# Kernel optimization log

Hardware: AMD Instinct MI355X
Metric: run time of the kernel (lower is better)

Reference implementation:

```python
import jax, jax.numpy as jnp
import numpy as np

N, B, D, T = 128, 512, 128, 16  # regions, batch, embed_dim, decode steps
C_CLIP = 10.0                   # tanh_clipping
NEG = -1e9


def setup_inputs() -> dict:
    key = jax.random.key(0)
    ks = jax.random.split(key, 40)
    s = 1.0 / np.sqrt(D)

    def w(k, shape):
        return jax.random.uniform(k, shape, jnp.float32, -s, s)

    return {
        'data': jax.random.normal(ks[0], (N, B, 4), jnp.float32),
        'node_embed': w(ks[1], (4, D)),
        'init_placeholder': w(ks[2], (D,)),
        'W1_w': w(ks[3], (D, D)), 'W1_b': w(ks[4], (D,)),
        'W2_w': w(ks[5], (D, D)), 'W2_b': w(ks[6], (D,)),
        'W3_w': w(ks[7], (D, D)), 'W3_b': w(ks[8], (D,)),
        'agg1_w': w(ks[9], (D, D)), 'agg1_b': w(ks[10], (D,)),
        'agg2_w': w(ks[11], (D, D)), 'agg2_b': w(ks[12], (D,)),
        'agg3_w': w(ks[13], (D, D)), 'agg3_b': w(ks[14], (D,)),
        'r1': jnp.ones((1,), jnp.float32),
        'r2': jnp.ones((1,), jnp.float32),
        'r3': jnp.ones((1,), jnp.float32),
        'lstm_Wih': w(ks[15], (4 * D, D)), 'lstm_Whh': w(ks[16], (4 * D, D)),
        'lstm_bih': w(ks[17], (4 * D,)), 'lstm_bhh': w(ks[18], (4 * D,)),
        'ptr_Wq': w(ks[19], (D, D)), 'ptr_bq': w(ks[20], (D,)),
        'ptr_Wref': w(ks[21], (D, D)), 'ptr_bref': w(ks[22], (D,)),
        'ptr_v': w(ks[23], (D,)),
        'glm_Wq': w(ks[24], (D, D)), 'glm_bq': w(ks[25], (D,)),
        'glm_Wref': w(ks[26], (D, D)), 'glm_bref': w(ks[27], (D,)),
        'glm_v': w(ks[28], (D,)),
    }


def _lin(x, w, b):
    return x @ w.T + b


def _attn_logits(q, e, Wq, bq, v):
    # q: [B,D], e: [B,D,N] (1x1-conv-projected ref). Bahdanau: v . tanh(Wq q + e)
    qq = (q @ Wq.T + bq)[:, :, None]          # [B,D,1]
    return jnp.einsum('d,bdn->bn', v, jnp.tanh(qq + e))  # [B,N]


def reference(data, node_embed, init_placeholder,
              W1_w, W1_b, W2_w, W2_b, W3_w, W3_b,
              agg1_w, agg1_b, agg2_w, agg2_b, agg3_w, agg3_b,
              r1, r2, r3,
              lstm_Wih, lstm_Whh, lstm_bih, lstm_bhh,
              ptr_Wq, ptr_bq, ptr_Wref, ptr_bref, ptr_v,
              glm_Wq, glm_bq, glm_Wref, glm_bref, glm_v):
    # node embedding: [N,B,4] @ [4,D] -> [N,B,D]
    emb = jnp.einsum('nbf,fd->nbd', data, node_embed)
    # GPN graph context: gated local transform + aggregated mean over nodes
    ctx = r1 * _lin(emb, W1_w, W1_b) + (1.0 - r1) * jax.nn.relu(_lin(emb.mean(0), agg1_w, agg1_b))
    ctx = r2 * _lin(ctx, W2_w, W2_b) + (1.0 - r2) * jax.nn.relu(_lin(ctx.mean(0), agg2_w, agg2_b))
    ctx = r3 * _lin(ctx, W3_w, W3_b) + (1.0 - r3) * jax.nn.relu(_lin(ctx.mean(0), agg3_w, agg3_b))
    # precompute 1x1-conv ref projections (ref is fixed over decode steps): [B,D,N]
    e_ptr = jnp.einsum('oi,nbi->bon', ptr_Wref, ctx) + ptr_bref[None, :, None]
    e_glm = jnp.einsum('oi,nbi->bon', glm_Wref, ctx) + glm_bref[None, :, None]
    emb_bnd = emb.transpose(1, 0, 2)  # [B,N,D] for gathering next decoder input

    def step(carry, _):
        h, c, x, visited = carry
        # LSTMCell (torch gate order i,f,g,o)
        gates = x @ lstm_Wih.T + lstm_bih + h @ lstm_Whh.T + lstm_bhh
        i, f, g, o = jnp.split(gates, 4, axis=-1)
        c = jax.nn.sigmoid(f) * c + jax.nn.sigmoid(i) * jnp.tanh(g)
        h = jax.nn.sigmoid(o) * jnp.tanh(c)
        # one glimpse (use_tanh=False), masked
        lg = _attn_logits(h, e_glm, glm_Wq, glm_bq, glm_v)
        lg = jnp.where(visited, NEG, lg)
        gl = jnp.einsum('bdn,bn->bd', e_glm, jax.nn.softmax(lg, axis=-1))
        # pointer (use_tanh=True, C=10), masked
        lp = C_CLIP * jnp.tanh(_attn_logits(gl, e_ptr, ptr_Wq, ptr_bq, ptr_v))
        lp = jnp.where(visited, NEG, lp)
        log_p = jax.nn.log_softmax(lp, axis=-1)  # temp = 1.0
        sel = jnp.argmax(log_p, axis=-1)         # greedy decode, [B]
        visited = visited | jax.nn.one_hot(sel, N, dtype=bool)
        x = jnp.take_along_axis(emb_bnd, sel[:, None, None], axis=1)[:, 0]  # [B,D]
        return (h, c, x, visited), log_p

    h0 = jnp.zeros((B, D), emb.dtype)
    c0 = jnp.zeros((B, D), emb.dtype)
    x0 = jnp.broadcast_to(init_placeholder, (B, D)).astype(emb.dtype)
    visited0 = jnp.zeros((B, N), bool)
    _, log_ps = jax.lax.scan(step, (h0, c0, x0, visited0), None, length=T)
    return log_ps  # [T,B,N]
```

## Files before the change

### kernel.cpp

```cpp
#include <hip/hip_runtime.h>
#include <math.h>


#define NREG   128
#define BATCH  512
#define DIM    128
#define TSTEPS 16
#define NEGV   (-1e9f)
#define LOG2E  1.4426950408889634f
#define CT     2.8853900817779268f

__device__ __forceinline__ float fexp2(float x) { return __builtin_amdgcn_exp2f(x); }
__device__ __forceinline__ float frcp(float x)  { return __builtin_amdgcn_rcpf(x); }
__device__ __forceinline__ float fast_tanh(float x) {
    return 1.f - 2.f * frcp(1.f + fexp2(CT * x));
}
__device__ __forceinline__ float fast_sig(float x) {
    return frcp(1.f + fexp2(-LOG2E * x));
}
__device__ __forceinline__ float fast_exp(float x) { return fexp2(LOG2E * x); }
__device__ __forceinline__ float fast_log(float x) {
    return __builtin_amdgcn_logf(x) * 0.6931471805599453f;
}

__device__ __forceinline__ float dot128(const float* __restrict__ wrow,
                                        const float* __restrict__ s) {
    float a0 = 0.f, a1 = 0.f, a2 = 0.f, a3 = 0.f;
#pragma unroll
    for (int k = 0; k < 128; k += 4) {
        a0 += wrow[k] * s[k];         a1 += wrow[k + 1] * s[k + 1];
        a2 += wrow[k + 2] * s[k + 2]; a3 += wrow[k + 3] * s[k + 3];
    }
    return (a0 + a1) + (a2 + a3);
}

__global__ __launch_bounds__(256) void k_misc(
    const float* __restrict__ Whh, const float* __restrict__ gWq,
    const float* __restrict__ Wih, const float* __restrict__ NE,
    const float* __restrict__ init_ph,
    const float* __restrict__ bih, const float* __restrict__ bhh,
    const float* __restrict__ W1, const float* __restrict__ b1,
    const float* __restrict__ W2, const float* __restrict__ b2,
    const float* __restrict__ W3, const float* __restrict__ b3,
    const float* __restrict__ a1w, const float* __restrict__ a1b,
    const float* __restrict__ a2w, const float* __restrict__ a2b,
    const float* __restrict__ a3w, const float* __restrict__ a3b,
    const float* __restrict__ gWr, const float* __restrict__ gbr,
    const float* __restrict__ pWr, const float* __restrict__ pbr,
    const float* __restrict__ pWq, const float* __restrict__ pbq,
    const float* __restrict__ r1p, const float* __restrict__ r2p,
    const float* __restrict__ r3p,
    const float* __restrict__ pv, const float* __restrict__ data,
    float* __restrict__ WhhP, float* __restrict__ gWqP,
    float* __restrict__ WihNE4, float* __restrict__ g0,
    float* __restrict__ bc, float* __restrict__ sumvp,
    float* __restrict__ Qgc, float* __restrict__ Qpc, float* __restrict__ GPQ,
    float* __restrict__ og, float* __restrict__ op, float* __restrict__ pog)
{
    __shared__ float Ws[128 * 129];
    __shared__ float me[1024], Cv[1024], Mv[1024], Tv[1024], C2[1024], M2[1024];
    __shared__ float NEs[512], mdS[32];
    __shared__ float4 Uc[128], Vc[128], Qgu[128];

    const int blk = blockIdx.x, t = threadIdx.x;

    if (blk < 64) {
        int idx = blk * 256 + t;
        int kb = idx >> 9, g = idx & 511;
        float4 v = *(const float4*)(Whh + g * 128 + kb * 4);
        ((float4*)WhhP)[kb * 512 + g] = v;
    } else if (blk < 80) {
        int idx = (blk - 64) * 256 + t;
        int ib = idx >> 7, o = idx & 127;
        float4 v = *(const float4*)(gWq + o * 128 + ib * 4);
        ((float4*)gWqP)[ib * 128 + o] = v;
    } else if (blk < 82) {
        int g = (blk - 80) * 256 + t;
        float a0 = 0.f, a1 = 0.f, a2 = 0.f, a3 = 0.f;
        for (int d = 0; d < 128; d += 4) {
            float4 wv = *(const float4*)(Wih + g * 128 + d);
            float4 n0 = *(const float4*)(NE + 0 * 128 + d);
            float4 n1 = *(const float4*)(NE + 1 * 128 + d);
            float4 n2 = *(const float4*)(NE + 2 * 128 + d);
            float4 n3 = *(const float4*)(NE + 3 * 128 + d);
            a0 += wv.x * n0.x + wv.y * n0.y + wv.z * n0.z + wv.w * n0.w;
            a1 += wv.x * n1.x + wv.y * n1.y + wv.z * n1.z + wv.w * n1.w;
            a2 += wv.x * n2.x + wv.y * n2.y + wv.z * n2.z + wv.w * n2.w;
            a3 += wv.x * n3.x + wv.y * n3.y + wv.z * n3.z + wv.w * n3.w;
        }
        *(float4*)(WihNE4 + g * 4) = make_float4(a0, a1, a2, a3);
    } else if (blk == 82) {
        for (int g = t; g < 512; g += 256) {
            float acc = 0.f;
            for (int d = 0; d < 128; d += 4) {
                float4 wv = *(const float4*)(Wih + g * 128 + d);
                float4 iv = *(const float4*)(init_ph + d);
                acc += wv.x * iv.x + wv.y * iv.y + wv.z * iv.z + wv.w * iv.w;
            }
            g0[g] = acc;
            bc[g] = bih[g] + bhh[g];
        }
        if (t < 64) {
            float sv = pv[t] + pv[t + 64];
            for (int off = 32; off; off >>= 1) sv += __shfl_xor(sv, off, 64);
            if (t == 0) sumvp[0] = sv;
        }
    } else if (blk == 83) {
        if (t < 128)
            Uc[t] = make_float4(NE[t], NE[128 + t], NE[256 + t], NE[384 + t]);
        __syncthreads();
#define CH_STAGE(Wp, SRC, DST, SC)                                             \
        if (t < 128) {                                                         \
            const float* wr = (Wp) + t * 128;                                  \
            float ax = 0.f, ay = 0.f, az = 0.f, aw = 0.f;                      \
            _Pragma("unroll 8")                                                \
            for (int k = 0; k < 128; k++) {                                    \
                float w = wr[k]; float4 u = SRC[k];                            \
                ax += w * u.x; ay += w * u.y; az += w * u.z; aw += w * u.w;    \
            }                                                                  \
            float sc = (SC);                                                   \
            DST[t] = make_float4(sc * ax, sc * ay, sc * az, sc * aw);          \
        }                                                                      \
        __syncthreads();
        CH_STAGE(W1, Uc, Vc, r1p[0])
        CH_STAGE(W2, Vc, Uc, r2p[0])
        CH_STAGE(W3, Uc, Vc, r3p[0])
        CH_STAGE(gWr, Vc, Qgu, 1.f)
        CH_STAGE(pWr, Vc, Uc, 1.f)
        CH_STAGE(pWq, Qgu, Vc, 1.f)
        if (t < 128) {
            float4 qg = Qgu[t], qp = Uc[t];
            ((float4*)Qgc)[t] = make_float4(CT * qg.x, CT * qg.y, CT * qg.z, CT * qg.w);
            ((float4*)Qpc)[t] = make_float4(CT * qp.x, CT * qp.y, CT * qp.z, CT * qp.w);
            ((float4*)GPQ)[t] = Vc[t];
        }
#undef CH_STAGE
    } else {
        const int b0 = (blk - 84) * 8;
        const float r1 = r1p[0], r2 = r2p[0], r3 = r3p[0];
#define STAGE_W(Wptr)                                                          \
        for (int i = t * 4; i < 16384; i += 1024) {                            \
            float4 v = *(const float4*)((Wptr) + i);                           \
            int oo = i >> 7, kk = i & 127;                                     \
            float* p = &Ws[oo * 129 + kk];                                     \
            p[0] = v.x; p[1] = v.y; p[2] = v.z; p[3] = v.w;                    \
        }
        if (t < 32) {
            int j = t >> 2, f = t & 3;
            float acc = 0.f;
            for (int n = 0; n < 128; n++) acc += data[n * 2048 + (b0 + j) * 4 + f];
            mdS[t] = acc * (1.f / 128.f);
        }
        for (int i = t; i < 512; i += 256) NEs[i] = NE[i];
        __syncthreads();
        for (int idx = t; idx < 1024; idx += 256) {
            int j = idx >> 7, d = idx & 127;
            me[idx] = mdS[j * 4 + 0] * NEs[d] + mdS[j * 4 + 1] * NEs[128 + d] +
                      mdS[j * 4 + 2] * NEs[256 + d] + mdS[j * 4 + 3] * NEs[384 + d];
        }
        STAGE_W(a1w);
        __syncthreads();
        {
            int o = t & 127, jg = t >> 7;
            for (int jj = 0; jj < 4; jj++) {
                int j = jg * 4 + jj;
                float acc = dot128(&Ws[o * 129], &me[j * 128]);
                Tv[j * 128 + o] = (1.f - r1) * fmaxf(acc + a1b[o], 0.f);
            }
        }
        __syncthreads();
        STAGE_W(W1);
        for (int idx = t; idx < 1024; idx += 256) Cv[idx] = r1 * b1[idx & 127] + Tv[idx];
        __syncthreads();
        {
            int o = t & 127, jg = t >> 7;
            for (int jj = 0; jj < 4; jj++) {
                int j = jg * 4 + jj;
                float acc = dot128(&Ws[o * 129], &me[j * 128]);
                Mv[j * 128 + o] = r1 * (acc + b1[o]) + Tv[j * 128 + o];
            }
        }
        __syncthreads();
        STAGE_W(a2w);
        __syncthreads();
        {
            int o = t & 127, jg = t >> 7;
            for (int jj = 0; jj < 4; jj++) {
                int j = jg * 4 + jj;
                float acc = dot128(&Ws[o * 129], &Mv[j * 128]);
                Tv[j * 128 + o] = (1.f - r2) * fmaxf(acc + a2b[o], 0.f);
            }
        }
        __syncthreads();
        STAGE_W(W2);
        __syncthreads();
        {
            int o = t & 127, jg = t >> 7;
            for (int jj = 0; jj < 4; jj++) {
                int j = jg * 4 + jj;
                float ac = dot128(&Ws[o * 129], &Cv[j * 128]);
                float am = dot128(&Ws[o * 129], &Mv[j * 128]);
                C2[j * 128 + o] = r2 * (ac + b2[o]) + Tv[j * 128 + o];
                M2[j * 128 + o] = r2 * (am + b2[o]) + Tv[j * 128 + o];
            }
        }
        __syncthreads();
        STAGE_W(a3w);
        __syncthreads();
        {
            int o = t & 127, jg = t >> 7;
            for (int jj = 0; jj < 4; jj++) {
                int j = jg * 4 + jj;
                float acc = dot128(&Ws[o * 129], &M2[j * 128]);
                Tv[j * 128 + o] = (1.f - r3) * fmaxf(acc + a3b[o], 0.f);
            }
        }
        __syncthreads();
        STAGE_W(W3);
        __syncthreads();
        {
            int o = t & 127, jg = t >> 7;
            for (int jj = 0; jj < 4; jj++) {
                int j = jg * 4 + jj;
                float acc = dot128(&Ws[o * 129], &C2[j * 128]);
                Cv[j * 128 + o] = r3 * (acc + b3[o]) + Tv[j * 128 + o];
            }
        }
        __syncthreads();
        STAGE_W(gWr);
        __syncthreads();
        {
            int o = t & 127, jg = t >> 7;
            for (int jj = 0; jj < 4; jj++) {
                int j = jg * 4 + jj;
                float acc = dot128(&Ws[o * 129], &Cv[j * 128]) + gbr[o];
                Mv[j * 128 + o] = acc;
                og[(long)(b0 + j) * 128 + o] = acc;
            }
        }
        __syncthreads();
        STAGE_W(pWr);
        __syncthreads();
        {
            int o = t & 127, jg = t >> 7;
            for (int jj = 0; jj < 4; jj++) {
                int j = jg * 4 + jj;
                op[(long)(b0 + j) * 128 + o] = dot128(&Ws[o * 129], &Cv[j * 128]) + pbr[o];
            }
        }
        __syncthreads();
        STAGE_W(pWq);
        __syncthreads();
        {
            int o = t & 127, jg = t >> 7;
            for (int jj = 0; jj < 4; jj++) {
                int j = jg * 4 + jj;
                pog[(long)(b0 + j) * 128 + o] = dot128(&Ws[o * 129], &Mv[j * 128]) + pbq[o];
            }
        }
#undef STAGE_W
    }
}

__global__ __launch_bounds__(512, 4) void k_decode(
    const float* __restrict__ dataIn,
    const float* __restrict__ WhhP,
    const float* __restrict__ gWqP,
    const float* __restrict__ WihNE4,
    const float* __restrict__ g0,
    const float* __restrict__ bc,
    const float* __restrict__ Qgc, const float* __restrict__ Qpc,
    const float* __restrict__ GPQ,
    const float* __restrict__ ogG, const float* __restrict__ opG,
    const float* __restrict__ pogG,
    const float* __restrict__ gbq, const float* __restrict__ vgG,
    const float* __restrict__ vpG, const float* __restrict__ sumvpG,
    float* __restrict__ out)
{
    __shared__ float4 dataS[128];
    __shared__ float4 WihS[512];
    __shared__ float4 QgcS[128], QpcS[128], GPQS[128];
    __shared__ float g0S[512], bcS[512], gatesS[512];
    __shared__ float ogS[128], opS[128], pogS[128];
    __shared__ float gbqS[128], vg2S[128], vp2S[128];
    __shared__ float hS[128], cS[128], qeS[128], qepS[128];
    __shared__ float lpart[4][128];
    __shared__ int   visitedS[128];
    __shared__ int   selS;
    __shared__ float sumvpS;

    const int t = threadIdx.x;
    const int b = blockIdx.x;

    if (t < 128) {
        dataS[t] = *(const float4*)(dataIn + ((long)t * 512 + b) * 4);
        QgcS[t]  = ((const float4*)Qgc)[t];
        QpcS[t]  = ((const float4*)Qpc)[t];
        GPQS[t]  = ((const float4*)GPQ)[t];
        ogS[t]   = ogG[(long)b * 128 + t];
        opS[t]   = opG[(long)b * 128 + t];
        pogS[t]  = pogG[(long)b * 128 + t];
        gbqS[t]  = gbq[t];
        vg2S[t]  = -2.f * vgG[t];
        vp2S[t]  = -2.f * vpG[t];
        hS[t] = 0.f; cS[t] = 0.f;
        visitedS[t] = 0;
    }
    WihS[t] = ((const float4*)WihNE4)[t];
    g0S[t] = g0[t];
    bcS[t] = bc[t];
    if (t == 0) sumvpS = sumvpG[0];
    __syncthreads();

    for (int step = 0; step < TSTEPS; step++) {
        {
            float ihp;
            if (step == 0) {
                ihp = g0S[t];
            } else {
                float4 xd = dataS[selS];
                float4 w = WihS[t];
                ihp = xd.x * w.x + xd.y * w.y + xd.z * w.z + xd.w * w.w;
            }
            ihp += bcS[t];
            const float4* wp = (const float4*)WhhP + t;
            float a0 = 0.f, a1 = 0.f, a2 = 0.f, a3 = 0.f;
#pragma unroll 8
            for (int kb = 0; kb < 32; kb++) {
                float4 w = wp[kb * 512];
                a0 += w.x * hS[4 * kb];     a1 += w.y * hS[4 * kb + 1];
                a2 += w.z * hS[4 * kb + 2]; a3 += w.w * hS[4 * kb + 3];
            }
            gatesS[t] = ihp + (a0 + a1) + (a2 + a3);
        }
        __syncthreads();
        if (t < 128) {
            float ig  = fast_sig(gatesS[t]);
            float fg  = fast_sig(gatesS[128 + t]);
            float gg  = fast_tanh(gatesS[256 + t]);
            float og_ = fast_sig(gatesS[384 + t]);
            float cn = fg * cS[t] + ig * gg;
            cS[t] = cn;
            hS[t] = og_ * fast_tanh(cn);
        }
        __syncthreads();
        if (t < 128) {
            const float4* wp = (const float4*)gWqP + t;
            float a0 = 0.f, a1 = 0.f, a2 = 0.f, a3 = 0.f;
#pragma unroll 8
            for (int ib = 0; ib < 32; ib++) {
                float4 w = wp[ib * 128];
                a0 += w.x * hS[4 * ib];     a1 += w.y * hS[4 * ib + 1];
                a2 += w.z * hS[4 * ib + 2]; a3 += w.w * hS[4 * ib + 3];
            }
            float q = (a0 + a1) + (a2 + a3) + gbqS[t];
            qeS[t] = CT * (q + ogS[t]);
        }
        __syncthreads();
        {
            int n = t & 127, q4 = t >> 7, d0 = q4 * 32;
            float4 dn = dataS[n];
            float acc = 0.f;
#pragma unroll 8
            for (int j = 0; j < 32; j++) {
                int d = d0 + j;
                float4 qg = QgcS[d];
                float x = qeS[d] + dn.x * qg.x + dn.y * qg.y + dn.z * qg.z + dn.w * qg.w;
                acc += vg2S[d] * frcp(1.f + fexp2(x));
            }
            lpart[q4][n] = acc;
        }
        __syncthreads();
        if (t < 64) {
            float l0 = visitedS[t] ? NEGV
                     : (lpart[0][t] + lpart[1][t]) + (lpart[2][t] + lpart[3][t]);
            float l1 = visitedS[t + 64] ? NEGV
                     : (lpart[0][t + 64] + lpart[1][t + 64]) + (lpart[2][t + 64] + lpart[3][t + 64]);
            float m = fmaxf(l0, l1);
            for (int off = 32; off; off >>= 1) m = fmaxf(m, __shfl_xor(m, off, 64));
            float p0 = fast_exp(l0 - m), p1 = fast_exp(l1 - m);
            float s = p0 + p1;
            float4 d0v = dataS[t], d1v = dataS[t + 64];
            float q0 = p0 * d0v.x + p1 * d1v.x;
            float q1 = p0 * d0v.y + p1 * d1v.y;
            float q2 = p0 * d0v.z + p1 * d1v.z;
            float q3 = p0 * d0v.w + p1 * d1v.w;
            for (int off = 32; off; off >>= 1) {
                s  += __shfl_xor(s, off, 64);
                q0 += __shfl_xor(q0, off, 64);
                q1 += __shfl_xor(q1, off, 64);
                q2 += __shfl_xor(q2, off, 64);
                q3 += __shfl_xor(q3, off, 64);
            }
            float inv = frcp(s);
            q0 *= inv; q1 *= inv; q2 *= inv; q3 *= inv;
            float4 gA = GPQS[t];
            qepS[t] = CT * (q0 * gA.x + q1 * gA.y + q2 * gA.z + q3 * gA.w
                            + pogS[t] + opS[t]);
            float4 gB = GPQS[t + 64];
            qepS[t + 64] = CT * (q0 * gB.x + q1 * gB.y + q2 * gB.z + q3 * gB.w
                                 + pogS[t + 64] + opS[t + 64]);
        }
        __syncthreads();
        {
            int n = t & 127, q4 = t >> 7, d0 = q4 * 32;
            float4 dn = dataS[n];
            float acc = 0.f;
#pragma unroll 8
            for (int j = 0; j < 32; j++) {
                int d = d0 + j;
                float4 qp = QpcS[d];
                float x = qepS[d] + dn.x * qp.x + dn.y * qp.y + dn.z * qp.z + dn.w * qp.w;
                acc += vp2S[d] * frcp(1.f + fexp2(x));
            }
            lpart[q4][n] = acc;
        }
        __syncthreads();
        if (t < 64) {
            float s0 = sumvpS + (lpart[0][t] + lpart[1][t]) + (lpart[2][t] + lpart[3][t]);
            float s1 = sumvpS + (lpart[0][t + 64] + lpart[1][t + 64])
                              + (lpart[2][t + 64] + lpart[3][t + 64]);
            float l0 = visitedS[t]      ? NEGV : 10.f * fast_tanh(s0);
            float l1 = visitedS[t + 64] ? NEGV : 10.f * fast_tanh(s1);
            float m = fmaxf(l0, l1);
            for (int off = 32; off; off >>= 1) m = fmaxf(m, __shfl_xor(m, off, 64));
            float p0 = fast_exp(l0 - m), p1 = fast_exp(l1 - m);
            float s = p0 + p1;
            for (int off = 32; off; off >>= 1) s += __shfl_xor(s, off, 64);
            float lse = m + fast_log(s);
            float* outp = out + ((long)step * BATCH + b) * NREG;
            outp[t] = l0 - lse;
            outp[t + 64] = l1 - lse;
            float v; int idx;
            if (l1 > l0) { v = l1; idx = t + 64; } else { v = l0; idx = t; }
            for (int off = 32; off; off >>= 1) {
                float ov = __shfl_xor(v, off, 64);
                int   oi = __shfl_xor(idx, off, 64);
                if (ov > v || (ov == v && oi < idx)) { v = ov; idx = oi; }
            }
            if (t == 0) { selS = idx; visitedS[idx] = 1; }
        }
        __syncthreads();
    }
}

extern "C" void kernel_launch(void* const* d_in, const int* in_sizes, int n_in,
                              void* d_out, int out_size, void* d_ws, size_t ws_size,
                              hipStream_t stream) {
    const float* data = (const float*)d_in[0];
    const float* NE   = (const float*)d_in[1];
    const float* init = (const float*)d_in[2];
    const float* W1w = (const float*)d_in[3];  const float* W1b = (const float*)d_in[4];
    const float* W2w = (const float*)d_in[5];  const float* W2b = (const float*)d_in[6];
    const float* W3w = (const float*)d_in[7];  const float* W3b = (const float*)d_in[8];
    const float* A1w = (const float*)d_in[9];  const float* A1b = (const float*)d_in[10];
    const float* A2w = (const float*)d_in[11]; const float* A2b = (const float*)d_in[12];
    const float* A3w = (const float*)d_in[13]; const float* A3b = (const float*)d_in[14];
    const float* r1  = (const float*)d_in[15];
    const float* r2  = (const float*)d_in[16];
    const float* r3  = (const float*)d_in[17];
    const float* Wih = (const float*)d_in[18]; const float* Whh = (const float*)d_in[19];
    const float* bih = (const float*)d_in[20]; const float* bhh = (const float*)d_in[21];
    const float* pWq = (const float*)d_in[22]; const float* pbq = (const float*)d_in[23];
    const float* pWr = (const float*)d_in[24]; const float* pbr = (const float*)d_in[25];
    const float* pv  = (const float*)d_in[26];
    const float* gWq = (const float*)d_in[27]; const float* gbq = (const float*)d_in[28];
    const float* gWr = (const float*)d_in[29]; const float* gbr = (const float*)d_in[30];
    const float* gv  = (const float*)d_in[31];
    float* out = (float*)d_out;

    float* ws     = (float*)d_ws;
    float* WhhP   = ws;
    float* gWqP   = WhhP + 65536;
    float* WihNE4 = gWqP + 16384;
    float* g0     = WihNE4 + 2048;
    float* bc     = g0 + 512;
    float* Qgc    = bc + 512;
    float* Qpc    = Qgc + 512;
    float* GPQ    = Qpc + 512;
    float* og     = GPQ + 512;
    float* op     = og + 65536;
    float* pog    = op + 65536;
    float* sumvp  = pog + 65536;

    k_misc<<<148, 256, 0, stream>>>(Whh, gWq, Wih, NE, init, bih, bhh,
                                    W1w, W1b, W2w, W2b, W3w, W3b,
                                    A1w, A1b, A2w, A2b, A3w, A3b,
                                    gWr, gbr, pWr, pbr, pWq, pbq,
                                    r1, r2, r3, pv, data,
                                    WhhP, gWqP, WihNE4, g0, bc, sumvp,
                                    Qgc, Qpc, GPQ, og, op, pog);
    k_decode<<<BATCH, 512, 0, stream>>>(data, WhhP, gWqP, WihNE4, g0, bc,
                                        Qgc, Qpc, GPQ, og, op, pog,
                                        gbq, gv, pv, sumvp, out);
}
```

Baseline: 366.5 us.

## Double decode block size and split LSTM and query matvecs across more threads

The decode kernel now launches 1024 threads per block instead of 512. The LSTM hidden matvec is split so each pair of threads handles half of a gate row, combined with a shuffle. The glimpse query matvec now uses 512 threads, four per output, reduced with shuffles, instead of 128. The aim is to shorten the serial per-step matvec latency by adding parallelism. In exchange there are more idle threads in the other phases, heavier __syncthreads, and the launch bound of 1024 with 8 blocks may force register pressure or limit occupancy.

```diff
diff --git a/kernel.cpp b/kernel.cpp
--- a/kernel.cpp
+++ b/kernel.cpp
@@ -262,7 +262,7 @@
     }
 }
 
-__global__ __launch_bounds__(512, 4) void k_decode(
+__global__ __launch_bounds__(1024, 8) void k_decode(
     const float* __restrict__ dataIn,
     const float* __restrict__ WhhP,
     const float* __restrict__ gWqP,
@@ -280,7 +280,7 @@
     __shared__ float4 dataS[128];
     __shared__ float4 WihS[512];
     __shared__ float4 QgcS[128], QpcS[128], GPQS[128];
-    __shared__ float g0S[512], bcS[512], gatesS[512];
+    __shared__ float g0S[512], bcS[512], gateS[512];
     __shared__ float ogS[128], opS[128], pogS[128];
     __shared__ float gbqS[128], vg2S[128], vp2S[128];
     __shared__ float hS[128], cS[128], qeS[128], qepS[128];
@@ -306,58 +306,66 @@
         hS[t] = 0.f; cS[t] = 0.f;
         visitedS[t] = 0;
     }
-    WihS[t] = ((const float4*)WihNE4)[t];
-    g0S[t] = g0[t];
-    bcS[t] = bc[t];
+    if (t < 512) {
+        WihS[t] = ((const float4*)WihNE4)[t];
+        g0S[t] = g0[t];
+        bcS[t] = bc[t];
+    }
     if (t == 0) sumvpS = sumvpG[0];
     __syncthreads();
 
     for (int step = 0; step < TSTEPS; step++) {
         {
-            float ihp;
-            if (step == 0) {
-                ihp = g0S[t];
-            } else {
-                float4 xd = dataS[selS];
-                float4 w = WihS[t];
-                ihp = xd.x * w.x + xd.y * w.y + xd.z * w.z + xd.w * w.w;
-            }
-            ihp += bcS[t];
-            const float4* wp = (const float4*)WhhP + t;
-            float a0 = 0.f, a1 = 0.f, a2 = 0.f, a3 = 0.f;
-#pragma unroll 8
+            int g = t >> 1, h2 = t & 1;
+            const float2* wp = (const float2*)WhhP + 2 * g + h2;
+            float a0 = 0.f, a1 = 0.f;
+#pragma unroll
             for (int kb = 0; kb < 32; kb++) {
-                float4 w = wp[kb * 512];
-                a0 += w.x * hS[4 * kb];     a1 += w.y * hS[4 * kb + 1];
-                a2 += w.z * hS[4 * kb + 2]; a3 += w.w * hS[4 * kb + 3];
-            }
-            gatesS[t] = ihp + (a0 + a1) + (a2 + a3);
+                float2 w = wp[(long)kb * 1024];
+                a0 += w.x * hS[4 * kb + 2 * h2];
+                a1 += w.y * hS[4 * kb + 2 * h2 + 1];
+            }
+            float part = a0 + a1;
+            float pb = __shfl_xor(part, 1);
+            if (h2 == 0) {
+                float ihp;
+                if (step == 0) {
+                    ihp = g0S[g];
+                } else {
+                    float4 xd = dataS[selS];
+                    float4 wv = WihS[g];
+                    ihp = xd.x * wv.x + xd.y * wv.y + xd.z * wv.z + xd.w * wv.w;
+                }
+                ihp += bcS[g];
+                gateS[g] = (ihp + part) + pb;
+            }
         }
         __syncthreads();
         if (t < 128) {
-            float ig  = fast_sig(gatesS[t]);
-            float fg  = fast_sig(gatesS[128 + t]);
-            float gg  = fast_tanh(gatesS[256 + t]);
-            float og_ = fast_sig(gatesS[384 + t]);
+            float ig  = fast_sig(gateS[t]);
+            float fg  = fast_sig(gateS[128 + t]);
+            float gg  = fast_tanh(gateS[256 + t]);
+            float og_ = fast_sig(gateS[384 + t]);
             float cn = fg * cS[t] + ig * gg;
             cS[t] = cn;
             hS[t] = og_ * fast_tanh(cn);
         }
         __syncthreads();
-        if (t < 128) {
-            const float4* wp = (const float4*)gWqP + t;
-            float a0 = 0.f, a1 = 0.f, a2 = 0.f, a3 = 0.f;
-#pragma unroll 8
-            for (int ib = 0; ib < 32; ib++) {
-                float4 w = wp[ib * 128];
-                a0 += w.x * hS[4 * ib];     a1 += w.y * hS[4 * ib + 1];
-                a2 += w.z * hS[4 * ib + 2]; a3 += w.w * hS[4 * ib + 3];
-            }
-            float q = (a0 + a1) + (a2 + a3) + gbqS[t];
-            qeS[t] = CT * (q + ogS[t]);
-        }
-        __syncthreads();
-        {
+        if (t < 512) {
+            int o = t >> 2, i = t & 3;
+            const float* wq = gWqP + o * 4 + i;
+            float a = 0.f;
+#pragma unroll
+            for (int ib = 0; ib < 32; ib++) a += wq[(long)ib * 512] * hS[4 * ib + i];
+            float r1v = a + __shfl_xor(a, 1);
+            float r2v = r1v + __shfl_xor(r1v, 2);
+            if (i == 0) {
+                float q = r2v + gbqS[o];
+                qeS[o] = CT * (q + ogS[o]);
+            }
+        }
+        __syncthreads();
+        if (t < 512) {
             int n = t & 127, q4 = t >> 7, d0 = q4 * 32;
             float4 dn = dataS[n];
             float acc = 0.f;
@@ -402,7 +410,7 @@
                                  + pogS[t + 64] + opS[t + 64]);
         }
         __syncthreads();
-        {
+        if (t < 512) {
             int n = t & 127, q4 = t >> 7, d0 = q4 * 32;
             float4 dn = dataS[n];
             float acc = 0.f;
@@ -490,7 +498,7 @@
                                     r1, r2, r3, pv, data,
                                     WhhP, gWqP, WihNE4, g0, bc, sumvp,
                                     Qgc, Qpc, GPQ, og, op, pog);
-    k_decode<<<BATCH, 512, 0, stream>>>(data, WhhP, gWqP, WihNE4, g0, bc,
-                                        Qgc, Qpc, GPQ, og, op, pog,
-                                        gbq, gv, pv, sumvp, out);
-}
+    k_decode<<<BATCH, 1024, 0, stream>>>(data, WhhP, gWqP, WihNE4, g0, bc,
+                                         Qgc, Qpc, GPQ, og, op, pog,
+                                         gbq, gv, pv, sumvp, out);
+}
```

Measured after the change: 839.3 us. 129% more time.
